# Optimization experiments

Measured on AMD Instinct MI355X. Metric: run time of the kernel, lower is better.

## Reference

```python
import jax, jax.numpy as jnp
import numpy as np

DIM = 1024
N_HEADS = 16
HEAD_DIM = DIM // N_HEADS
FREQS = [31.0, 37.0, 41.0, 43.0, 47.0]
TWO_PI = 2.0 * float(np.pi)


def setup_inputs() -> dict:
    key = jax.random.key(0)
    ks = jax.random.split(key, 16)
    B, L = 2, 1024
    s = 0.02
    inp = {
        'x': jax.random.normal(ks[0], (B, L, DIM), dtype=jnp.float32),
        'Wq': jax.random.normal(ks[1], (DIM, DIM), dtype=jnp.float32) * s,
        'bq': jnp.zeros((DIM,), dtype=jnp.float32),
        'Wk': jax.random.normal(ks[2], (DIM, DIM), dtype=jnp.float32) * s,
        'bk': jnp.zeros((DIM,), dtype=jnp.float32),
        'Wv': jax.random.normal(ks[3], (DIM, DIM), dtype=jnp.float32) * s,
        'bv': jnp.zeros((DIM,), dtype=jnp.float32),
        'Wo': jax.random.normal(ks[4], (DIM, DIM), dtype=jnp.float32) * s,
        'bo': jnp.zeros((DIM,), dtype=jnp.float32),
        'alpha': jax.random.normal(ks[5], (N_HEADS, len(FREQS)), dtype=jnp.float32) * 0.1,
        'phi': jax.random.uniform(ks[6], (N_HEADS, len(FREQS)), dtype=jnp.float32) * TWO_PI,
        'temperature': jnp.ones((1,), dtype=jnp.float32),
        'gamma': jnp.ones((DIM,), dtype=jnp.float32),
        'beta': jnp.zeros((DIM,), dtype=jnp.float32),
    }
    return inp


def reference(x, Wq, bq, Wk, bk, Wv, bv, Wo, bo, alpha, phi, temperature, gamma, beta):
    B, L, D = x.shape
    H, hd = N_HEADS, HEAD_DIM
    # projections (torch Linear: y = x @ W.T + b), split heads -> (B,H,L,hd)
    q = (x @ Wq.T + bq).reshape(B, L, H, hd).transpose(0, 2, 1, 3)
    k = (x @ Wk.T + bk).reshape(B, L, H, hd).transpose(0, 2, 1, 3)
    v = (x @ Wv.T + bv).reshape(B, L, H, hd).transpose(0, 2, 1, 3)
    # similarity (B,H,L,L)
    sim = jnp.einsum('bhid,bhjd->bhij', q, k) / jnp.sqrt(jnp.asarray(hd, x.dtype))
    temp = jnp.abs(temperature)[0] + 0.1
    sim = sim / temp
    # multi-frequency holographic scores: sum_f alpha_f * sin(2*pi*sim/p_f + phi_f)
    scores = jnp.zeros_like(sim)
    for fi, freq in enumerate(FREQS):
        a = alpha[:, fi][None, :, None, None]
        p = phi[:, fi][None, :, None, None]
        scores = scores + a * jnp.sin(TWO_PI * sim / freq + p)
    # sigmoid-sum normalization (not softmax)
    w = jax.nn.sigmoid(scores)
    w = w / (jnp.sum(w, axis=-1, keepdims=True) + 1e-10)
    out = jnp.einsum('bhij,bhjd->bhid', w, v)
    out = out.transpose(0, 2, 1, 3).reshape(B, L, D)
    out = out @ Wo.T + bo
    # LayerNorm (eps=1e-5, biased variance)
    mu = jnp.mean(out, axis=-1, keepdims=True)
    var = jnp.mean(jnp.square(out - mu), axis=-1, keepdims=True)
    return (out - mu) / jnp.sqrt(var + 1e-5) * gamma + beta
```

## Files before the change

### kernel.cpp

```cpp
#include <hip/hip_runtime.h>
#include <hip/hip_bf16.h>

typedef short bf16x8 __attribute__((ext_vector_type(8)));
typedef float f32x4 __attribute__((ext_vector_type(4)));

#define MFMA16(a, b, c) __builtin_amdgcn_mfma_f32_16x16x32_bf16(a, b, c, 0, 0, 0)

static constexpr int SEQ = 1024;
static constexpr int DIM = 1024;
static constexpr int NH = 16;
static constexpr int HD = 64;

#if __has_builtin(__builtin_amdgcn_rcpf)
#define FAST_RCP(x) __builtin_amdgcn_rcpf(x)
#else
#define FAST_RCP(x) (1.0f / (x))
#endif

#if __has_builtin(__builtin_amdgcn_exp2f)
#define EXP2F(x) __builtin_amdgcn_exp2f(x)
#else
#define EXP2F(x) exp2f(x)
#endif

__device__ __forceinline__ int swz(int r) { return r ^ (r >> 3); }

__device__ __forceinline__ void gload16(const __hip_bfloat16* g, __hip_bfloat16* l)
{
    typedef const __attribute__((address_space(1))) unsigned GU;
    typedef __attribute__((address_space(3))) unsigned LU;
    __builtin_amdgcn_global_load_lds((GU*)g, (LU*)l, 16, 0, 0);
}

__device__ __forceinline__ unsigned pack2bf(float a, float b)
{
    union { __hip_bfloat16 h; unsigned short u; } ca, cb;
    ca.h = __float2bfloat16(a); cb.h = __float2bfloat16(b);
    return (unsigned)ca.u | ((unsigned)cb.u << 16);
}

__global__ __launch_bounds__(256) void cvt_all(
    const float* __restrict__ x,  const float* __restrict__ wq,
    const float* __restrict__ wk, const float* __restrict__ wv,
    const float* __restrict__ wo,
    __hip_bfloat16* __restrict__ xb,  __hip_bfloat16* __restrict__ wqb,
    __hip_bfloat16* __restrict__ wkb, __hip_bfloat16* __restrict__ wvb,
    __hip_bfloat16* __restrict__ wob)
{
    const int reg = blockIdx.y;
    const float* src; __hip_bfloat16* dst; int n;
    if      (reg == 0) { src = x;  dst = xb;  n = 2 * SEQ * DIM; }
    else if (reg == 1) { src = wq; dst = wqb; n = DIM * DIM; }
    else if (reg == 2) { src = wk; dst = wkb; n = DIM * DIM; }
    else if (reg == 3) { src = wv; dst = wvb; n = DIM * DIM; }
    else               { src = wo; dst = wob; n = DIM * DIM; }
    const int i = (blockIdx.x * 256 + threadIdx.x) * 4;
    if (i < n) {
        float4 v = *(const float4*)(src + i);
        __hip_bfloat16 t[4];
        t[0] = __float2bfloat16(v.x); t[1] = __float2bfloat16(v.y);
        t[2] = __float2bfloat16(v.z); t[3] = __float2bfloat16(v.w);
        *(ushort4*)(dst + i) = *(ushort4*)t;
    }
}

__global__ __launch_bounds__(256) void gemm_qkv(
    const __hip_bfloat16* __restrict__ A,
    const __hip_bfloat16* __restrict__ W0, const __hip_bfloat16* __restrict__ W1,
    const __hip_bfloat16* __restrict__ W2,
    const float* __restrict__ b0, const float* __restrict__ b1,
    const float* __restrict__ b2,
    __hip_bfloat16* __restrict__ Y0, __hip_bfloat16* __restrict__ Y1,
    __hip_bfloat16* __restrict__ Y2,
    int M, int N, int K)
{
    __shared__ __align__(16) __hip_bfloat16 As[64 * 64];
    __shared__ __align__(16) __hip_bfloat16 Ws[128 * 64];

    const int z = blockIdx.z;
    const __hip_bfloat16* W = (z == 0) ? W0 : ((z == 1) ? W1 : W2);
    const float* bias = (z == 0) ? b0 : ((z == 1) ? b1 : b2);
    __hip_bfloat16* Y = (z == 0) ? Y0 : ((z == 1) ? Y1 : Y2);

    const int tid = threadIdx.x;
    const int wv = tid >> 6, lane = tid & 63;
    const int col16 = lane & 15, quad = lane >> 4;
    const int m0 = blockIdx.x * 64, n0 = blockIdx.y * 128;
    const int wr = wv >> 1, wc = wv & 1;

    const int scol = ((tid & 7) ^ ((tid >> 3) & 7)) * 8;
    const __hip_bfloat16* ga = A + (size_t)(m0 + (tid >> 3)) * K + scol;
    const __hip_bfloat16* gb = W + (size_t)(n0 + (tid >> 3)) * K + scol;
    __hip_bfloat16* lA = As + wv * 512;
    __hip_bfloat16* lB = Ws + wv * 512;

    const int c7 = col16 & 7;
    const int so0 = ((quad)     ^ c7) * 8;
    const int so1 = ((quad + 4) ^ c7) * 8;
    const __hip_bfloat16* ar = As + (wr * 32 + col16) * 64;
    const __hip_bfloat16* br = Ws + (wc * 64 + col16) * 64;

    f32x4 acc[8] = {};

    for (int k0 = 0; k0 < K; k0 += 64) {
        gload16(ga + k0,                  lA);
        gload16(ga + k0 + (size_t)32 * K, lA + 2048);
        gload16(gb + k0,                  lB);
        gload16(gb + k0 + (size_t)32 * K, lB + 2048);
        gload16(gb + k0 + (size_t)64 * K, lB + 4096);
        gload16(gb + k0 + (size_t)96 * K, lB + 6144);
        __syncthreads();
#pragma unroll
        for (int kh = 0; kh < 2; ++kh) {
            const int so = (kh == 0) ? so0 : so1;
            bf16x8 af[2], bfm[4];
#pragma unroll
            for (int mt = 0; mt < 2; ++mt) af[mt] = *(const bf16x8*)(ar + mt * 16 * 64 + so);
#pragma unroll
            for (int nt = 0; nt < 4; ++nt) bfm[nt] = *(const bf16x8*)(br + nt * 16 * 64 + so);
#pragma unroll
            for (int mt = 0; mt < 2; ++mt)
#pragma unroll
                for (int nt = 0; nt < 4; ++nt)
                    acc[mt * 4 + nt] = MFMA16(af[mt], bfm[nt], acc[mt * 4 + nt]);
        }
        __syncthreads();
    }

#pragma unroll
    for (int nt = 0; nt < 4; ++nt) {
        const int n = n0 + wc * 64 + nt * 16 + col16;
        const float bv = bias[n];
#pragma unroll
        for (int mt = 0; mt < 2; ++mt) {
#pragma unroll
            for (int r = 0; r < 4; ++r) {
                const int m = m0 + wr * 32 + mt * 16 + quad * 4 + r;
                Y[(size_t)m * N + n] = __float2bfloat16(acc[mt * 4 + nt][r] + bv);
            }
        }
    }
}

__global__ __launch_bounds__(256) void gemm_osplit(
    const __hip_bfloat16* __restrict__ A,
    const __hip_bfloat16* __restrict__ W,
    const float* __restrict__ bias,
    float* __restrict__ Y0, float* __restrict__ Y1,
    int M, int N, int K)
{
    __shared__ __align__(16) __hip_bfloat16 As[64 * 64];
    __shared__ __align__(16) __hip_bfloat16 Ws[128 * 64];

    const int z = blockIdx.z;
    float* Y = (z == 0) ? Y0 : Y1;
    const int kb = z * 512;

    const int tid = threadIdx.x;
    const int wv = tid >> 6, lane = tid & 63;
    const int col16 = lane & 15, quad = lane >> 4;
    const int m0 = blockIdx.x * 64, n0 = blockIdx.y * 128;
    const int wr = wv >> 1, wc = wv & 1;

    const int scol = ((tid & 7) ^ ((tid >> 3) & 7)) * 8;
    const __hip_bfloat16* ga = A + (size_t)(m0 + (tid >> 3)) * K + scol + kb;
    const __hip_bfloat16* gb = W + (size_t)(n0 + (tid >> 3)) * K + scol + kb;
    __hip_bfloat16* lA = As + wv * 512;
    __hip_bfloat16* lB = Ws + wv * 512;

    const int c7 = col16 & 7;
    const int so0 = ((quad)     ^ c7) * 8;
    const int so1 = ((quad + 4) ^ c7) * 8;
    const __hip_bfloat16* ar = As + (wr * 32 + col16) * 64;
    const __hip_bfloat16* br = Ws + (wc * 64 + col16) * 64;

    f32x4 acc[8] = {};

    for (int k0 = 0; k0 < 512; k0 += 64) {
        gload16(ga + k0,                  lA);
        gload16(ga + k0 + (size_t)32 * K, lA + 2048);
        gload16(gb + k0,                  lB);
        gload16(gb + k0 + (size_t)32 * K, lB + 2048);
        gload16(gb + k0 + (size_t)64 * K, lB + 4096);
        gload16(gb + k0 + (size_t)96 * K, lB + 6144);
        __syncthreads();
#pragma unroll
        for (int kh = 0; kh < 2; ++kh) {
            const int so = (kh == 0) ? so0 : so1;
            bf16x8 af[2], bfm[4];
#pragma unroll
            for (int mt = 0; mt < 2; ++mt) af[mt] = *(const bf16x8*)(ar + mt * 16 * 64 + so);
#pragma unroll
            for (int nt = 0; nt < 4; ++nt) bfm[nt] = *(const bf16x8*)(br + nt * 16 * 64 + so);
#pragma unroll
            for (int mt = 0; mt < 2; ++mt)
#pragma unroll
                for (int nt = 0; nt < 4; ++nt)
                    acc[mt * 4 + nt] = MFMA16(af[mt], bfm[nt], acc[mt * 4 + nt]);
        }
        __syncthreads();
    }

#pragma unroll
    for (int nt = 0; nt < 4; ++nt) {
        const int n = n0 + wc * 64 + nt * 16 + col16;
        const float bv = (z == 0) ? bias[n] : 0.0f;
#pragma unroll
        for (int mt = 0; mt < 2; ++mt) {
#pragma unroll
            for (int r = 0; r < 4; ++r) {
                const int m = m0 + wr * 32 + mt * 16 + quad * 4 + r;
                Y[(size_t)m * N + n] = acc[mt * 4 + nt][r] + bv;
            }
        }
    }
}

__global__ __launch_bounds__(256) void attn_kernel(
    const __hip_bfloat16* __restrict__ Q,
    const __hip_bfloat16* __restrict__ K,
    const __hip_bfloat16* __restrict__ V,
    const float* __restrict__ alpha, const float* __restrict__ phi,
    const float* __restrict__ temperature,
    __hip_bfloat16* __restrict__ AO)
{
    __shared__ __align__(16) char smem[18432 + 512];
    __hip_bfloat16* VtBase = (__hip_bfloat16*)smem;
    float* Ocomb = (float*)smem;
    float* Dl    = (float*)(smem + 2 * 16 * 68 * 4);

    const int tid = threadIdx.x;
    const int wv = tid >> 6, lane = tid & 63;
    const int col16 = lane & 15, quad = lane >> 4;
    const int g = wv & 1, half = wv >> 1;

    const int bh = blockIdx.y, b = bh >> 4, h = bh & 15;
    const int i0 = blockIdx.x * 32 + g * 16;
    const size_t base = ((size_t)b * SEQ) * DIM + (size_t)h * HD;

    const float tempv = fabsf(temperature[0]) + 0.1f;
    const float simscale = 1.0f / (8.0f * tempv);
    const float freqs[5] = {31.0f, 37.0f, 41.0f, 43.0f, 47.0f};

    float p[8] = {0.f, 0.f, 0.f, 0.f, 0.f, 0.f, 0.f, 0.f};
#pragma unroll
    for (int f = 0; f < 5; ++f) {
        const float a  = alpha[h * 5 + f] * 1.44269504089f;
        const float ph = phi[h * 5 + f];
        const float sp = __sinf(ph), cp = __cosf(ph);
        const float c  = 6.28318530718f * simscale / freqs[f];
        const float c2 = c * c, c3 = c2 * c, c4 = c2 * c2;
        const float c5 = c4 * c, c6 = c4 * c2, c7 = c4 * c3;
        p[0] += a * sp;
        p[1] += a * cp * c;
        p[2] -= a * sp * c2 * 0.5f;
        p[3] -= a * cp * c3 * (1.0f / 6.0f);
        p[4] += a * sp * c4 * (1.0f / 24.0f);
        p[5] += a * cp * c5 * (1.0f / 120.0f);
        p[6] -= a * sp * c6 * (1.0f / 720.0f);
        p[7] -= a * cp * c7 * (1.0f / 5040.0f);
    }

    const __hip_bfloat16* qrow = Q + base + (size_t)(i0 + col16) * DIM + quad * 8;
    const bf16x8 qa0 = *(const bf16x8*)(qrow);
    const bf16x8 qa1 = *(const bf16x8*)(qrow + 32);

    const __hip_bfloat16* kbase = K + base + (size_t)col16 * DIM + quad * 8;

    const int tl = tid & 127;
    const int sc0 = (tl & 7) * 8;
    const int sx  = tl & 7;
    const int jj0 = (tl >> 3) * 2;
    const int pu = (jj0 >> 4) & 1, pqs = (jj0 >> 2) & 3, pr = jj0 & 3;
    const int col0 = ((pqs ^ (pu << 1)) << 3) + (pu << 2) + pr;
    __hip_bfloat16* VtH = VtBase + half * 64 * 72;
    __hip_bfloat16* rowp[8];
#pragma unroll
    for (int e = 0; e < 8; ++e) rowp[e] = VtH + (sc0 + (e ^ sx)) * 72;

    const __hip_bfloat16* vrd[4];
#pragma unroll
    for (int t = 0; t < 4; ++t)
        vrd[t] = VtH + swz(t * 16 + col16) * 72 + quad * 8;

    f32x4 o[4] = {};
    float denomL = 0.f;

    bf16x8 vr[2][2];
    bf16x8 kf[4][2];

    {
        const int j0 = half * 512;
#pragma unroll
        for (int s = 0; s < 2; ++s) {
            const __hip_bfloat16* vp = V + base + (size_t)(j0 + jj0 + 32 * s) * DIM + sc0;
            vr[s][0] = *(const bf16x8*)(vp);
            vr[s][1] = *(const bf16x8*)(vp + DIM);
        }
#pragma unroll
        for (int u = 0; u < 4; ++u) {
            const __hip_bfloat16* kp = kbase + (size_t)(j0 + u * 16) * DIM;
            kf[u][0] = *(const bf16x8*)(kp);
            kf[u][1] = *(const bf16x8*)(kp + 32);
        }
    }

    for (int it = 0; it < 8; ++it) {
        __syncthreads();
#pragma unroll
        for (int s = 0; s < 2; ++s) {
#pragma unroll
            for (int e = 0; e < 8; ++e) {
                unsigned pk = ((unsigned)(unsigned short)vr[s][0][e]) |
                              (((unsigned)(unsigned short)vr[s][1][e]) << 16);
                *(unsigned*)(rowp[e] + col0 + 32 * s) = pk;
            }
        }
        __syncthreads();

        const int j1 = half * 512 + (it + 1) * 64;
        if (it < 7) {
#pragma unroll
            for (int s = 0; s < 2; ++s) {
                const __hip_bfloat16* vp = V + base + (size_t)(j1 + jj0 + 32 * s) * DIM + sc0;
                vr[s][0] = *(const bf16x8*)(vp);
                vr[s][1] = *(const bf16x8*)(vp + DIM);
            }
        }

        f32x4 sa4[4];
        __builtin_amdgcn_s_setprio(1);
#pragma unroll
        for (int u = 0; u < 4; ++u) {
            f32x4 zz = {};
            zz = MFMA16(kf[u][0], qa0, zz);
            zz = MFMA16(kf[u][1], qa1, zz);
            sa4[u] = zz;
        }
        __builtin_amdgcn_s_setprio(0);

        if (it < 7) {
#pragma unroll
            for (int u = 0; u < 4; ++u) {
                const __hip_bfloat16* kp = kbase + (size_t)(j1 + u * 16) * DIM;
                kf[u][0] = *(const bf16x8*)(kp);
                kf[u][1] = *(const bf16x8*)(kp + 32);
            }
        }

#pragma unroll
        for (int sub = 0; sub < 2; ++sub) {
            float w[2][4];
#pragma unroll
            for (int s2 = 0; s2 < 2; ++s2) {
                const int u = sub * 2 + s2;
#pragma unroll
                for (int r = 0; r < 4; ++r) {
                    const float sv = sa4[u][r];
                    float sc = fmaf(sv, p[7], p[6]);
                    sc = fmaf(sv, sc, p[5]);
                    sc = fmaf(sv, sc, p[4]);
                    sc = fmaf(sv, sc, p[3]);
                    sc = fmaf(sv, sc, p[2]);
                    sc = fmaf(sv, sc, p[1]);
                    sc = fmaf(sv, sc, p[0]);
                    const float ww = FAST_RCP(1.0f + EXP2F(-sc));
                    denomL += ww;
                    w[s2][r] = ww;
                }
            }
            const unsigned pk00 = pack2bf(w[0][0], w[0][1]);
            const unsigned pk01 = pack2bf(w[0][2], w[0][3]);
            const unsigned pk10 = pack2bf(w[1][0], w[1][1]);
            const unsigned pk11 = pack2bf(w[1][2], w[1][3]);
            const unsigned sw0 = (unsigned)__shfl_xor((int)pk10, 32);
            const unsigned sw1 = (unsigned)__shfl_xor((int)pk11, 32);
            union { unsigned d[4]; bf16x8 v; } pu8;
            pu8.d[0] = pk00; pu8.d[1] = pk01; pu8.d[2] = sw0; pu8.d[3] = sw1;
            const bf16x8 pa = pu8.v;

            __builtin_amdgcn_s_setprio(1);
#pragma unroll
            for (int t = 0; t < 4; ++t) {
                bf16x8 vb = *(const bf16x8*)(vrd[t] + 32 * sub);
                o[t] = MFMA16(pa, vb, o[t]);
            }
            __builtin_amdgcn_s_setprio(0);
        }
    }

    denomL += __shfl_xor(denomL, 16);
    denomL += __shfl_xor(denomL, 32);

    __syncthreads();
    if (quad == 0) Dl[half * 32 + g * 16 + col16] = denomL;
    if (half == 1) {
#pragma unroll
        for (int t = 0; t < 4; ++t)
#pragma unroll
            for (int r = 0; r < 4; ++r)
                Ocomb[(g * 16 + quad * 4 + r) * 68 + t * 16 + col16] = o[t][r];
    }
    __syncthreads();
    if (half == 0) {
        float dn[4];
#pragma unroll
        for (int r = 0; r < 4; ++r)
            dn[r] = Dl[g * 16 + quad * 4 + r] + Dl[32 + g * 16 + quad * 4 + r] + 1e-10f;
#pragma unroll
        for (int t = 0; t < 4; ++t) {
#pragma unroll
            for (int r = 0; r < 4; ++r) {
                const float val =
                    (o[t][r] + Ocomb[(g * 16 + quad * 4 + r) * 68 + t * 16 + col16]) / dn[r];
                const size_t row = (size_t)b * SEQ + i0 + quad * 4 + r;
                AO[row * DIM + h * HD + t * 16 + col16] = __float2bfloat16(val);
            }
        }
    }
}

__global__ __launch_bounds__(256) void ln_kernel(
    const float* __restrict__ Yp0,
    const float* __restrict__ Yp1,
    const float* __restrict__ gamma,
    const float* __restrict__ beta,
    float* __restrict__ out)
{
    const int row = blockIdx.x;
    const float* y0 = Yp0 + (size_t)row * DIM;
    const float* y1 = Yp1 + (size_t)row * DIM;

    float v[4];
    float s = 0.f, s2 = 0.f;
#pragma unroll
    for (int e = 0; e < 4; ++e) {
        const int idx = threadIdx.x + e * 256;
        v[e] = y0[idx] + y1[idx];
        s += v[e];
        s2 += v[e] * v[e];
    }
#pragma unroll
    for (int off = 1; off < 64; off <<= 1) {
        s  += __shfl_xor(s, off);
        s2 += __shfl_xor(s2, off);
    }
    __shared__ float ps[4], ps2[4];
    const int wave = threadIdx.x >> 6;
    if ((threadIdx.x & 63) == 0) { ps[wave] = s; ps2[wave] = s2; }
    __syncthreads();
    s  = ps[0] + ps[1] + ps[2] + ps[3];
    s2 = ps2[0] + ps2[1] + ps2[2] + ps2[3];

    const float mu   = s * (1.0f / DIM);
    const float var  = s2 * (1.0f / DIM) - mu * mu;
    const float rstd = rsqrtf(var + 1e-5f);

#pragma unroll
    for (int e = 0; e < 4; ++e) {
        const int idx = threadIdx.x + e * 256;
        out[(size_t)row * DIM + idx] =
            (v[e] - mu) * rstd * gamma[idx] + beta[idx];
    }
}

extern "C" void kernel_launch(void* const* d_in, const int* in_sizes, int n_in,
                              void* d_out, int out_size, void* d_ws, size_t ws_size,
                              hipStream_t stream)
{
    const float* x     = (const float*)d_in[0];
    const float* Wq    = (const float*)d_in[1];
    const float* bq    = (const float*)d_in[2];
    const float* Wk    = (const float*)d_in[3];
    const float* bk    = (const float*)d_in[4];
    const float* Wv    = (const float*)d_in[5];
    const float* bv    = (const float*)d_in[6];
    const float* Wo    = (const float*)d_in[7];
    const float* bo    = (const float*)d_in[8];
    const float* alpha = (const float*)d_in[9];
    const float* phi   = (const float*)d_in[10];
    const float* temp  = (const float*)d_in[11];
    const float* gamma = (const float*)d_in[12];
    const float* beta  = (const float*)d_in[13];

    float* out = (float*)d_out;

    const int B = 2;
    const int M = B * SEQ;

    char* wsb = (char*)d_ws;
    __hip_bfloat16* xb  = (__hip_bfloat16*)(wsb + 0);
    __hip_bfloat16* Wqb = (__hip_bfloat16*)(wsb + (4u  << 20));
    __hip_bfloat16* Wkb = (__hip_bfloat16*)(wsb + (6u  << 20));
    __hip_bfloat16* Wvb = (__hip_bfloat16*)(wsb + (8u  << 20));
    __hip_bfloat16* Wob = (__hip_bfloat16*)(wsb + (10u << 20));
    __hip_bfloat16* Qb  = (__hip_bfloat16*)(wsb + (12u << 20));
    __hip_bfloat16* Kb  = (__hip_bfloat16*)(wsb + (16u << 20));
    __hip_bfloat16* Vb  = (__hip_bfloat16*)(wsb + (20u << 20));
    __hip_bfloat16* AO  = (__hip_bfloat16*)(wsb + (24u << 20));
    float*          Yp0 = (float*)(wsb + 0);
    float*          Yp1 = (float*)(wsb + (12u << 20));

    hipLaunchKernelGGL(cvt_all, dim3(2048, 5), dim3(256), 0, stream,
                       x, Wq, Wk, Wv, Wo, xb, Wqb, Wkb, Wvb, Wob);

    hipLaunchKernelGGL(gemm_qkv, dim3(M / 64, DIM / 128, 3), dim3(256), 0, stream,
                       xb, Wqb, Wkb, Wvb, bq, bk, bv, Qb, Kb, Vb, M, DIM, DIM);

    hipLaunchKernelGGL(attn_kernel, dim3(SEQ / 32, B * NH), dim3(256), 0, stream,
                       Qb, Kb, Vb, alpha, phi, temp, AO);

    hipLaunchKernelGGL(gemm_osplit, dim3(M / 64, DIM / 128, 2), dim3(256), 0, stream,
                       AO, Wob, bo, Yp0, Yp1, M, DIM, DIM);

    hipLaunchKernelGGL(ln_kernel, dim3(M), dim3(256), 0, stream,
                       Yp0, Yp1, gamma, beta, out);
}
```

Baseline: 169.6 us.

## Double-buffer LDS tiles in GEMMs and attention V staging

The QKV and output-projection GEMMs now use two LDS buffers, loading the next K tile while MFMAs run on the current one, so each iteration needs one barrier instead of two. The attention kernel double-buffers the transposed V tile, writing the next tile to the alternate buffer and prefetching V two steps ahead, again with one barrier per iteration. The aim is to hide global-load and LDS-write latency. In exchange LDS use doubles and register pressure rises, which may lower occupancy.

```diff
diff --git a/kernel.cpp b/kernel.cpp
--- a/kernel.cpp
+++ b/kernel.cpp
@@ -74,8 +74,8 @@
     __hip_bfloat16* __restrict__ Y2,
     int M, int N, int K)
 {
-    __shared__ __align__(16) __hip_bfloat16 As[64 * 64];
-    __shared__ __align__(16) __hip_bfloat16 Ws[128 * 64];
+    __shared__ __align__(16) __hip_bfloat16 As[2][64 * 64];
+    __shared__ __align__(16) __hip_bfloat16 Ws[2][128 * 64];
 
     const int z = blockIdx.z;
     const __hip_bfloat16* W = (z == 0) ? W0 : ((z == 1) ? W1 : W2);
@@ -91,25 +91,34 @@
     const int scol = ((tid & 7) ^ ((tid >> 3) & 7)) * 8;
     const __hip_bfloat16* ga = A + (size_t)(m0 + (tid >> 3)) * K + scol;
     const __hip_bfloat16* gb = W + (size_t)(n0 + (tid >> 3)) * K + scol;
-    __hip_bfloat16* lA = As + wv * 512;
-    __hip_bfloat16* lB = Ws + wv * 512;
+    const int wofs = wv * 512;
 
     const int c7 = col16 & 7;
     const int so0 = ((quad)     ^ c7) * 8;
     const int so1 = ((quad + 4) ^ c7) * 8;
-    const __hip_bfloat16* ar = As + (wr * 32 + col16) * 64;
-    const __hip_bfloat16* br = Ws + (wc * 64 + col16) * 64;
+
+#define QKV_STAGE(k0, buf)                                         \
+    {                                                              \
+        __hip_bfloat16* lA = As[buf] + wofs;                       \
+        __hip_bfloat16* lB = Ws[buf] + wofs;                       \
+        gload16(ga + (k0),                    lA);                 \
+        gload16(ga + (k0) + (size_t)32 * K,   lA + 2048);          \
+        gload16(gb + (k0),                    lB);                 \
+        gload16(gb + (k0) + (size_t)32 * K,   lB + 2048);          \
+        gload16(gb + (k0) + (size_t)64 * K,   lB + 4096);          \
+        gload16(gb + (k0) + (size_t)96 * K,   lB + 6144);          \
+    }
+
+    QKV_STAGE(0, 0);
+    __syncthreads();
 
     f32x4 acc[8] = {};
-
-    for (int k0 = 0; k0 < K; k0 += 64) {
-        gload16(ga + k0,                  lA);
-        gload16(ga + k0 + (size_t)32 * K, lA + 2048);
-        gload16(gb + k0,                  lB);
-        gload16(gb + k0 + (size_t)32 * K, lB + 2048);
-        gload16(gb + k0 + (size_t)64 * K, lB + 4096);
-        gload16(gb + k0 + (size_t)96 * K, lB + 6144);
-        __syncthreads();
+    const int NT = K / 64;
+    for (int t = 0; t < NT; ++t) {
+        const int buf = t & 1;
+        if (t + 1 < NT) QKV_STAGE((t + 1) * 64, buf ^ 1);
+        const __hip_bfloat16* ar = As[buf] + (wr * 32 + col16) * 64;
+        const __hip_bfloat16* br = Ws[buf] + (wc * 64 + col16) * 64;
 #pragma unroll
         for (int kh = 0; kh < 2; ++kh) {
             const int so = (kh == 0) ? so0 : so1;
@@ -126,6 +135,7 @@
         }
         __syncthreads();
     }
+#undef QKV_STAGE
 
 #pragma unroll
     for (int nt = 0; nt < 4; ++nt) {
@@ -149,8 +159,8 @@
     float* __restrict__ Y0, float* __restrict__ Y1,
     int M, int N, int K)
 {
-    __shared__ __align__(16) __hip_bfloat16 As[64 * 64];
-    __shared__ __align__(16) __hip_bfloat16 Ws[128 * 64];
+    __shared__ __align__(16) __hip_bfloat16 As[2][64 * 64];
+    __shared__ __align__(16) __hip_bfloat16 Ws[2][128 * 64];
 
     const int z = blockIdx.z;
     float* Y = (z == 0) ? Y0 : Y1;
@@ -165,25 +175,33 @@
     const int scol = ((tid & 7) ^ ((tid >> 3) & 7)) * 8;
     const __hip_bfloat16* ga = A + (size_t)(m0 + (tid >> 3)) * K + scol + kb;
     const __hip_bfloat16* gb = W + (size_t)(n0 + (tid >> 3)) * K + scol + kb;
-    __hip_bfloat16* lA = As + wv * 512;
-    __hip_bfloat16* lB = Ws + wv * 512;
+    const int wofs = wv * 512;
 
     const int c7 = col16 & 7;
     const int so0 = ((quad)     ^ c7) * 8;
     const int so1 = ((quad + 4) ^ c7) * 8;
-    const __hip_bfloat16* ar = As + (wr * 32 + col16) * 64;
-    const __hip_bfloat16* br = Ws + (wc * 64 + col16) * 64;
+
+#define OS_STAGE(k0, buf)                                          \
+    {                                                              \
+        __hip_bfloat16* lA = As[buf] + wofs;                       \
+        __hip_bfloat16* lB = Ws[buf] + wofs;                       \
+        gload16(ga + (k0),                    lA);                 \
+        gload16(ga + (k0) + (size_t)32 * K,   lA + 2048);          \
+        gload16(gb + (k0),                    lB);                 \
+        gload16(gb + (k0) + (size_t)32 * K,   lB + 2048);          \
+        gload16(gb + (k0) + (size_t)64 * K,   lB + 4096);          \
+        gload16(gb + (k0) + (size_t)96 * K,   lB + 6144);          \
+    }
+
+    OS_STAGE(0, 0);
+    __syncthreads();
 
     f32x4 acc[8] = {};
-
-    for (int k0 = 0; k0 < 512; k0 += 64) {
-        gload16(ga + k0,                  lA);
-        gload16(ga + k0 + (size_t)32 * K, lA + 2048);
-        gload16(gb + k0,                  lB);
-        gload16(gb + k0 + (size_t)32 * K, lB + 2048);
-        gload16(gb + k0 + (size_t)64 * K, lB + 4096);
-        gload16(gb + k0 + (size_t)96 * K, lB + 6144);
-        __syncthreads();
+    for (int t = 0; t < 8; ++t) {
+        const int buf = t & 1;
+        if (t + 1 < 8) OS_STAGE((t + 1) * 64, buf ^ 1);
+        const __hip_bfloat16* ar = As[buf] + (wr * 32 + col16) * 64;
+        const __hip_bfloat16* br = Ws[buf] + (wc * 64 + col16) * 64;
 #pragma unroll
         for (int kh = 0; kh < 2; ++kh) {
             const int so = (kh == 0) ? so0 : so1;
@@ -200,6 +218,7 @@
         }
         __syncthreads();
     }
+#undef OS_STAGE
 
 #pragma unroll
     for (int nt = 0; nt < 4; ++nt) {
@@ -224,10 +243,10 @@
     const float* __restrict__ temperature,
     __hip_bfloat16* __restrict__ AO)
 {
-    __shared__ __align__(16) char smem[18432 + 512];
+    __shared__ __align__(16) char smem[2 * 18432 + 512];
     __hip_bfloat16* VtBase = (__hip_bfloat16*)smem;
     float* Ocomb = (float*)smem;
-    float* Dl    = (float*)(smem + 2 * 16 * 68 * 4);
+    float* Dl    = (float*)(smem + 2 * 18432);
 
     const int tid = threadIdx.x;
     const int wv = tid >> 6, lane = tid & 63;
@@ -273,7 +292,7 @@
     const int jj0 = (tl >> 3) * 2;
     const int pu = (jj0 >> 4) & 1, pqs = (jj0 >> 2) & 3, pr = jj0 & 3;
     const int col0 = ((pqs ^ (pu << 1)) << 3) + (pu << 2) + pr;
-    __hip_bfloat16* VtH = VtBase + half * 64 * 72;
+    __hip_bfloat16* VtH = VtBase + half * 4608;
     __hip_bfloat16* rowp[8];
 #pragma unroll
     for (int e = 0; e < 8; ++e) rowp[e] = VtH + (sc0 + (e ^ sx)) * 72;
@@ -289,14 +308,36 @@
     bf16x8 vr[2][2];
     bf16x8 kf[4][2];
 
+#define LOADV(jt)                                                              \
+    {                                                                          \
+        const int jv = half * 512 + (jt) * 64;                                 \
+        _Pragma("unroll")                                                      \
+        for (int s = 0; s < 2; ++s) {                                          \
+            const __hip_bfloat16* vp =                                         \
+                V + base + (size_t)(jv + jj0 + 32 * s) * DIM + sc0;            \
+            vr[s][0] = *(const bf16x8*)(vp);                                   \
+            vr[s][1] = *(const bf16x8*)(vp + DIM);                             \
+        }                                                                      \
+    }
+
+#define PACKV(pofs)                                                            \
+    {                                                                          \
+        _Pragma("unroll")                                                      \
+        for (int s = 0; s < 2; ++s) {                                          \
+            _Pragma("unroll")                                                  \
+            for (int e = 0; e < 8; ++e) {                                      \
+                unsigned pk = ((unsigned)(unsigned short)vr[s][0][e]) |        \
+                              (((unsigned)(unsigned short)vr[s][1][e]) << 16); \
+                *(unsigned*)(rowp[e] + (pofs) + col0 + 32 * s) = pk;           \
+            }                                                                  \
+        }                                                                      \
+    }
+
+    LOADV(0);
+    PACKV(0);
+    LOADV(1);
     {
         const int j0 = half * 512;
-#pragma unroll
-        for (int s = 0; s < 2; ++s) {
-            const __hip_bfloat16* vp = V + base + (size_t)(j0 + jj0 + 32 * s) * DIM + sc0;
-            vr[s][0] = *(const bf16x8*)(vp);
-            vr[s][1] = *(const bf16x8*)(vp + DIM);
-        }
 #pragma unroll
         for (int u = 0; u < 4; ++u) {
             const __hip_bfloat16* kp = kbase + (size_t)(j0 + u * 16) * DIM;
@@ -304,29 +345,12 @@
             kf[u][1] = *(const bf16x8*)(kp + 32);
         }
     }
+    __syncthreads();
 
     for (int it = 0; it < 8; ++it) {
-        __syncthreads();
-#pragma unroll
-        for (int s = 0; s < 2; ++s) {
-#pragma unroll
-            for (int e = 0; e < 8; ++e) {
-                unsigned pk = ((unsigned)(unsigned short)vr[s][0][e]) |
-                              (((unsigned)(unsigned short)vr[s][1][e]) << 16);
-                *(unsigned*)(rowp[e] + col0 + 32 * s) = pk;
-            }
-        }
-        __syncthreads();
-
-        const int j1 = half * 512 + (it + 1) * 64;
-        if (it < 7) {
-#pragma unroll
-            for (int s = 0; s < 2; ++s) {
-                const __hip_bfloat16* vp = V + base + (size_t)(j1 + jj0 + 32 * s) * DIM + sc0;
-                vr[s][0] = *(const bf16x8*)(vp);
-                vr[s][1] = *(const bf16x8*)(vp + DIM);
-            }
-        }
+        const int cur = it & 1;
+        if (it < 7) PACKV((cur ^ 1) * 9216);
+        if (it < 6) LOADV(it + 2);
 
         f32x4 sa4[4];
         __builtin_amdgcn_s_setprio(1);
@@ -340,6 +364,7 @@
         __builtin_amdgcn_s_setprio(0);
 
         if (it < 7) {
+            const int j1 = half * 512 + (it + 1) * 64;
 #pragma unroll
             for (int u = 0; u < 4; ++u) {
                 const __hip_bfloat16* kp = kbase + (size_t)(j1 + u * 16) * DIM;
@@ -382,17 +407,19 @@
             __builtin_amdgcn_s_setprio(1);
 #pragma unroll
             for (int t = 0; t < 4; ++t) {
-                bf16x8 vb = *(const bf16x8*)(vrd[t] + 32 * sub);
+                bf16x8 vb = *(const bf16x8*)(vrd[t] + cur * 9216 + 32 * sub);
                 o[t] = MFMA16(pa, vb, o[t]);
             }
             __builtin_amdgcn_s_setprio(0);
         }
-    }
+        __syncthreads();
+    }
+#undef LOADV
+#undef PACKV
 
     denomL += __shfl_xor(denomL, 16);
     denomL += __shfl_xor(denomL, 32);
 
-    __syncthreads();
     if (quad == 0) Dl[half * 32 + g * 16 + col16] = denomL;
     if (half == 1) {
 #pragma unroll
```

Result: no change. 169.8 us (+0.1%).
